# Kernel optimization log

Hardware: AMD Instinct MI355X
Metric: run time of the kernel (lower is better)

The kernel has to match this reference:

```python
import jax, jax.numpy as jnp
import numpy as np

B, L, D_IN, H, FEAT, PROJ = 1024, 128, 130, 768, 49, 40


def setup_inputs() -> dict:
    key = jax.random.key(0)
    ks = jax.random.split(key, 16)
    s = 0.05
    return {
        "X": jax.random.normal(ks[0], (B, L, D_IN), dtype=jnp.float32),
        "Fe": jax.random.normal(ks[1], (B, FEAT), dtype=jnp.float32),
        # three attention heads densa1/2/3 stacked: [3, H, L]
        "W_att": jax.random.normal(ks[2], (3, H, L), dtype=jnp.float32) * s,
        "b_att": jax.random.normal(ks[3], (3, L), dtype=jnp.float32) * s,
        # LSTMCell(3*D_IN, H) params, PyTorch layout
        "W_ih": jax.random.normal(ks[4], (4 * H, 3 * D_IN), dtype=jnp.float32) * s,
        "W_hh": jax.random.normal(ks[5], (4 * H, H), dtype=jnp.float32) * s,
        "b_ih": jax.random.normal(ks[6], (4 * H,), dtype=jnp.float32) * s,
        "b_hh": jax.random.normal(ks[7], (4 * H,), dtype=jnp.float32) * s,
        # Dense1: Linear(H, FEAT)
        "W_d1": jax.random.normal(ks[8], (FEAT, H), dtype=jnp.float32) * s,
        "b_d1": jax.random.normal(ks[9], (FEAT,), dtype=jnp.float32) * s,
        # AttFeat R: Linear(FEAT, PROJ); A: Linear(PROJ, 1, bias=False)
        "W_r": jax.random.normal(ks[10], (PROJ, FEAT), dtype=jnp.float32) * s,
        "b_r": jax.random.normal(ks[11], (PROJ,), dtype=jnp.float32) * s,
        "W_a": jax.random.normal(ks[12], (1, PROJ), dtype=jnp.float32) * s,
        # Dense2: Linear(PROJ, 2)
        "W_d2": jax.random.normal(ks[13], (2, PROJ), dtype=jnp.float32) * s,
        "b_d2": jax.random.normal(ks[14], (2,), dtype=jnp.float32) * s,
    }


def reference(X, Fe, W_att, b_att, W_ih, W_hh, b_ih, b_hh, W_d1, b_d1, W_r, b_r, W_a, W_d2, b_d2):
    b = X.shape[0]

    def step(carry, _):
        h, c = carry
        # three softmax attention distributions over the sequence: [b, 3, L]
        logits = jnp.einsum('bh,khl->bkl', h, W_att) + b_att
        alp = jax.nn.softmax(logits, axis=-1)
        # weighted sums over seq -> concat of v1,v2,v3: [b, 3*D_IN]
        v = jnp.einsum('bkl,bld->bkd', alp, X).reshape(b, -1)
        # PyTorch LSTMCell update
        gates = v @ W_ih.T + b_ih + h @ W_hh.T + b_hh
        i, f, g, o = jnp.split(gates, 4, axis=-1)
        c_new = jax.nn.sigmoid(f) * c + jax.nn.sigmoid(i) * jnp.tanh(g)
        h_new = jax.nn.sigmoid(o) * jnp.tanh(c_new)
        return (h_new, c_new), h_new

    h0 = jnp.zeros((b, H), dtype=X.dtype)
    c0 = jnp.zeros((b, H), dtype=X.dtype)
    _, hs = jax.lax.scan(step, (h0, c0), None, length=L)  # [L, b, H]
    out = jnp.transpose(hs, (1, 0, 2))                    # [b, L, H]

    # MaxLayer: max-pool over the sequence dim
    x = jnp.max(out, axis=1)                              # [b, H]

    # Dense1 + ReLU
    y = jax.nn.relu(x @ W_d1.T + b_d1)                    # [b, FEAT]

    # AttFeat over [y, Fe]
    r1 = jax.nn.leaky_relu(y @ W_r.T + b_r)               # [b, PROJ]
    r2 = jax.nn.leaky_relu(Fe @ W_r.T + b_r)
    a1 = jnp.tanh(r1) @ W_a.T                             # [b, 1]
    a2 = jnp.tanh(r2) @ W_a.T
    a = jax.nn.softmax(jnp.concatenate([a1, a2], axis=-1), axis=-1)  # [b, 2]
    s = jax.nn.relu(a[:, 0:1] * r1 + a[:, 1:2] * r2)      # [b, PROJ]

    # Dense2 (squeeze is a no-op for b > 1)
    return s @ W_d2.T + b_d2                              # [b, 2]
```

## Files before the change

kernel.cpp:

```cpp
#include <hip/hip_runtime.h>
#include <stdint.h>


#define B_SZ   1024
#define LSEQ   128
#define DIN    130
#define HDIM   768
#define NFEAT  49
#define NPROJ  40
#define KPAD   1216
#define VOFF   416
#define NGATE  3072
#define KT_G   19
#define XELEM  (LSEQ * DIN)
#define GBUF   20480

typedef unsigned short u16;
typedef __attribute__((ext_vector_type(8))) short short8;
typedef __attribute__((ext_vector_type(4))) float f32x4;

__device__ __forceinline__ u16 f2bf(float f) {
  unsigned int u = __float_as_uint(f);
  u += 0x7FFFu + ((u >> 16) & 1u);
  return (u16)(u >> 16);
}
__device__ __forceinline__ float bf2f(u16 b) {
  return __uint_as_float(((unsigned int)b) << 16);
}
__device__ __forceinline__ float frcp(float x) {
  return __builtin_amdgcn_rcpf(x);
}
__device__ __forceinline__ float ftanh(float x) {
  return 1.f - 2.f * frcp(1.f + __expf(2.f * x));
}
__device__ __forceinline__ float fsigm(float x) {
  return frcp(1.f + __expf(-x));
}
__device__ __forceinline__ void gload16(const void* g, void* l) {
  __builtin_amdgcn_global_load_lds(
      (__attribute__((address_space(1))) const void*)g,
      (__attribute__((address_space(3))) void*)l, 16, 0, 0);
}

__global__ __launch_bounds__(256, 4) void gemm_logits_k(
    const u16* __restrict__ Ah,
    const u16* __restrict__ Bh, float* __restrict__ Cp)
{
  __shared__ __align__(16) u16 sAh[32 * 40];
  __shared__ __align__(16) u16 sBh[64 * 40];

  const int tid = threadIdx.x, lane = tid & 63, wid = tid >> 6;
  const int wm = (wid & 1) * 16, wn = (wid >> 1) * 32;
  const int lm = lane & 15, quad = lane >> 4;
  const int bm = blockIdx.x * 32, bn = blockIdx.y * 64;
  const int kh = blockIdx.z;
  const int kbase = kh * 384;
  float* __restrict__ C = Cp + (size_t)kh * B_SZ * 384;

  const bool aload = tid < 128;
  const int ar = tid >> 2, ac = (tid & 3) * 8;
  const size_t a_off = (size_t)(bm + ar) * KPAD + kbase + ac;
  const size_t b_off = (size_t)(bn + ar) * HDIM + kbase + ac;

  uint4 ph, pb;
  if (aload) ph = *(const uint4*)(Ah + a_off);
  pb = *(const uint4*)(Bh + b_off);

  f32x4 acc0 = {0.f, 0.f, 0.f, 0.f}, acc1 = {0.f, 0.f, 0.f, 0.f};

  for (int kt = 0; kt < 12; ++kt) {
    if (aload) *(uint4*)&sAh[ar * 40 + ac] = ph;
    *(uint4*)&sBh[ar * 40 + ac] = pb;
    __syncthreads();
    if (kt + 1 < 12) {
      const int k0 = (kt + 1) * 32;
      if (aload) ph = *(const uint4*)(Ah + a_off + k0);
      pb = *(const uint4*)(Bh + b_off + k0);
    }
    const short8 ah = *(const short8*)&sAh[(wm + lm) * 40 + quad * 8];
    const short8 b0 = *(const short8*)&sBh[(wn + lm) * 40 + quad * 8];
    const short8 b1 = *(const short8*)&sBh[(wn + 16 + lm) * 40 + quad * 8];
    acc0 = __builtin_amdgcn_mfma_f32_16x16x32_bf16(ah, b0, acc0, 0, 0, 0);
    acc1 = __builtin_amdgcn_mfma_f32_16x16x32_bf16(ah, b1, acc1, 0, 0, 0);
    __syncthreads();
  }

  const int col = bn + wn + lm;
  const int row0 = bm + wm + quad * 4;
#pragma unroll
  for (int r = 0; r < 4; ++r) {
    C[(size_t)(row0 + r) * 384 + col]      = acc0[r];
    C[(size_t)(row0 + r) * 384 + col + 16] = acc1[r];
  }
}

__global__ __launch_bounds__(256, 2) void gates_lstm(
    const u16* __restrict__ Ah,
    const u16* __restrict__ Wh,
    const float* __restrict__ bsum,
    float* __restrict__ cst, float* __restrict__ hmax,
    u16* __restrict__ out_h)
{
  __shared__ __align__(16) char smem[3 * GBUF];

  const int tid = threadIdx.x, lane = tid & 63, wid = tid >> 6;
  const int wm = (wid >> 1) * 32, wn = (wid & 1) * 48;
  const int lm = lane & 15, quad = lane >> 4;

  const int wg = blockIdx.x;
  const int vid = (wg & 7) * 64 + (wg >> 3);
  const int bm = (vid & 15) * 64;
  const int j0 = (vid >> 4) * 24;

  const u16* Asrc[2];
#pragma unroll
  for (int i = 0; i < 2; ++i) {
    const int r = i * 32 + wid * 8 + (lane >> 3);
    const int s = (lane & 7) ^ (r & 7);
    Asrc[i] = Ah + (size_t)(bm + r) * KPAD + (s << 3);
  }
  const u16* Bsrc[3];
#pragma unroll
  for (int i = 0; i < 3; ++i) {
    const int r = i * 32 + wid * 8 + (lane >> 3);
    const int s = (lane & 7) ^ (r & 7);
    const int nrow = (r / 24) * HDIM + j0 + (r % 24);
    Bsrc[i] = Wh + (size_t)nrow * KPAD + (s << 3);
  }

  int aoff[2], boff[3];
#pragma unroll
  for (int mi = 0; mi < 2; ++mi) {
    const int R = wm + mi * 16 + lm;
    aoff[mi] = R * 64 + ((quad ^ (R & 7)) << 3);
  }
#pragma unroll
  for (int ni = 0; ni < 3; ++ni) {
    const int R = wn + ni * 16 + lm;
    boff[ni] = R * 64 + ((quad ^ (R & 7)) << 3);
  }

  f32x4 acc[2][3];
#pragma unroll
  for (int mi = 0; mi < 2; ++mi)
#pragma unroll
    for (int ni = 0; ni < 3; ++ni) acc[mi][ni] = (f32x4){0.f, 0.f, 0.f, 0.f};

  auto stage = [&](int buf, int kt) {
    char* bb = smem + buf * GBUF;
    const int k0 = kt * 64;
#pragma unroll
    for (int i = 0; i < 2; ++i)
      gload16(Asrc[i] + k0, bb + ((i << 12) + (wid << 10)));
#pragma unroll
    for (int i = 0; i < 3; ++i)
      gload16(Bsrc[i] + k0, bb + 8192 + ((i << 12) + (wid << 10)));
  };

  stage(0, 0);
  stage(1, 1);

  int cur = 0;
  for (int kt = 0; kt < KT_G; ++kt) {
    if (kt + 2 < KT_G) {
      int nbuf = cur + 2; if (nbuf >= 3) nbuf -= 3;
      stage(nbuf, kt + 2);
      asm volatile("s_waitcnt vmcnt(10)" ::: "memory");
    } else if (kt + 1 < KT_G) {
      asm volatile("s_waitcnt vmcnt(5)" ::: "memory");
    } else {
      asm volatile("s_waitcnt vmcnt(0)" ::: "memory");
    }
    asm volatile("s_barrier" ::: "memory");

    const u16* sA = (const u16*)(smem + cur * GBUF);
    const u16* sB = sA + 4096;
#pragma unroll
    for (int kk = 0; kk < 2; ++kk) {
      const int kx = kk << 5;
      short8 af[2], bg[3];
#pragma unroll
      for (int mi = 0; mi < 2; ++mi)
        af[mi] = *(const short8*)(sA + (aoff[mi] ^ kx));
#pragma unroll
      for (int ni = 0; ni < 3; ++ni)
        bg[ni] = *(const short8*)(sB + (boff[ni] ^ kx));
#pragma unroll
      for (int mi = 0; mi < 2; ++mi)
#pragma unroll
        for (int ni = 0; ni < 3; ++ni)
          acc[mi][ni] = __builtin_amdgcn_mfma_f32_16x16x32_bf16(
              af[mi], bg[ni], acc[mi][ni], 0, 0, 0);
    }
    asm volatile("s_barrier" ::: "memory");
    cur += 1; if (cur >= 3) cur -= 3;
  }

  float* tile = (float*)smem;
#pragma unroll
  for (int mi = 0; mi < 2; ++mi)
#pragma unroll
    for (int ni = 0; ni < 3; ++ni) {
      const int c = wn + ni * 16 + lm;
#pragma unroll
      for (int r = 0; r < 4; ++r)
        tile[(wm + mi * 16 + quad * 4 + r) * 100 + c] = acc[mi][ni][r];
    }
  __syncthreads();

#pragma unroll
  for (int i = 0; i < 6; ++i) {
    const int lin = tid + 256 * i;
    const int row = lin / 24, jj = lin - row * 24;
    const int b = bm + row, j = j0 + jj;
    const float* tr = tile + row * 100;
    const float pi = tr[jj]      + bsum[j];
    const float pf = tr[24 + jj] + bsum[HDIM + j];
    const float pg = tr[48 + jj] + bsum[2 * HDIM + j];
    const float po = tr[72 + jj] + bsum[3 * HDIM + j];
    const float si = fsigm(pi);
    const float sf = fsigm(pf);
    const float so = fsigm(po);
    const size_t cidx = (size_t)b * HDIM + j;
    const float cn = sf * cst[cidx] + si * ftanh(pg);
    const float hn = so * ftanh(cn);
    cst[cidx] = cn;
    hmax[cidx] = fmaxf(hmax[cidx], hn);
    out_h[(size_t)b * KPAD + VOFF + j] = f2bf(hn);
  }
}

__global__ __launch_bounds__(512, 4) void softmax_v(
    const float* __restrict__ l0, const float* __restrict__ l1,
    const float* __restrict__ b_att,
    const u16* __restrict__ XT,
    u16* __restrict__ act)
{
  const int b = blockIdx.x;
  const int t = threadIdx.x;
  __shared__ __align__(16) u16 sXT[XELEM];
  __shared__ __align__(16) float s_alp[384];
  __shared__ float s_w[16];

  {
    const uint4* src = (const uint4*)(XT + (size_t)b * XELEM);
    uint4* dst = (uint4*)sXT;
#pragma unroll
    for (int rep = 0; rep < 4; ++rep) {
      const int i = t + rep * 512;
      const int d = i >> 4, blk = i & 15;
      dst[d * 16 + (blk ^ (d & 7))] = src[i];
    }
    if (t < 32) {
      const int i = 2048 + t;
      const int d = i >> 4, blk = i & 15;
      dst[d * 16 + (blk ^ (d & 7))] = src[i];
    }
  }

  const int lane = t & 63, wv = t >> 6, hw = wv & ~1;
  float x = -3.4e38f;
  if (t < 384)
    x = l0[(size_t)b * 384 + t] + l1[(size_t)b * 384 + t] + b_att[t];

  float m = x;
#pragma unroll
  for (int off = 32; off > 0; off >>= 1) m = fmaxf(m, __shfl_xor(m, off));
  if (lane == 0 && wv < 6) s_w[wv] = m;
  __syncthreads();

  float e = 0.f;
  if (t < 384) e = __expf(x - fmaxf(s_w[hw], s_w[hw | 1]));
  float sum = e;
#pragma unroll
  for (int off = 32; off > 0; off >>= 1) sum += __shfl_xor(sum, off);
  if (lane == 0 && wv < 6) s_w[8 + wv] = sum;
  __syncthreads();

  if (t < 384) {
    const float sk = s_w[8 + hw] + s_w[8 + (hw | 1)];
    s_alp[t] = e * frcp(sk);
  }
  __syncthreads();

  if (t < 390) {
    const int k = t / 130;
    const int d = t - k * 130;
    const uint4* xr = (const uint4*)sXT;
    const int dbase = d * 16, dsw = d & 7;
    const float* ab = s_alp + (k << 7);
    float acc = 0.f;
#pragma unroll
    for (int c = 0; c < 16; ++c) {
      const uint4 raw = xr[dbase + (c ^ dsw)];
      const float4 a0 = *(const float4*)(ab + (c << 3));
      const float4 a1 = *(const float4*)(ab + (c << 3) + 4);
      acc += a0.x * bf2f((u16)(raw.x & 0xffff));
      acc += a0.y * bf2f((u16)(raw.x >> 16));
      acc += a0.z * bf2f((u16)(raw.y & 0xffff));
      acc += a0.w * bf2f((u16)(raw.y >> 16));
      acc += a1.x * bf2f((u16)(raw.z & 0xffff));
      acc += a1.y * bf2f((u16)(raw.z >> 16));
      acc += a1.z * bf2f((u16)(raw.w & 0xffff));
      acc += a1.w * bf2f((u16)(raw.w >> 16));
    }
    act[(size_t)b * KPAD + t] = f2bf(acc);
  }
}

__global__ __launch_bounds__(64) void final_head(
    const float* __restrict__ hmax, const float* __restrict__ Fe,
    const float* __restrict__ W_d1, const float* __restrict__ b_d1,
    const float* __restrict__ W_r,  const float* __restrict__ b_r,
    const float* __restrict__ W_a,
    const float* __restrict__ W_d2, const float* __restrict__ b_d2,
    float* __restrict__ out)
{
  const int b = blockIdx.x;
  const int t = threadIdx.x;
  __shared__ float sx[HDIM];
  __shared__ float sy[NFEAT];
  __shared__ float sr1[NPROJ], sr2[NPROJ];
  __shared__ float sa[2];

  for (int i = t; i < HDIM; i += 64) sx[i] = hmax[(size_t)b * HDIM + i];
  __syncthreads();

  if (t < NFEAT) {
    float acc = b_d1[t];
    const float* w = W_d1 + (size_t)t * HDIM;
    for (int i = 0; i < HDIM; ++i) acc += sx[i] * w[i];
    sy[t] = fmaxf(acc, 0.f);
  }
  __syncthreads();

  if (t < NPROJ) {
    float a1 = b_r[t], a2 = b_r[t];
    const float* w  = W_r + (size_t)t * NFEAT;
    const float* fe = Fe + (size_t)b * NFEAT;
    for (int i = 0; i < NFEAT; ++i) { a1 += sy[i] * w[i]; a2 += fe[i] * w[i]; }
    sr1[t] = (a1 > 0.f) ? a1 : 0.01f * a1;
    sr2[t] = (a2 > 0.f) ? a2 : 0.01f * a2;
  }
  __syncthreads();

  if (t == 0) {
    float a1 = 0.f, a2 = 0.f;
    for (int p = 0; p < NPROJ; ++p) {
      a1 += tanhf(sr1[p]) * W_a[p];
      a2 += tanhf(sr2[p]) * W_a[p];
    }
    const float mx = fmaxf(a1, a2);
    const float e1 = expf(a1 - mx), e2 = expf(a2 - mx);
    sa[0] = e1 / (e1 + e2);
    sa[1] = e2 / (e1 + e2);
  }
  __syncthreads();

  if (t < 2) {
    float acc = b_d2[t];
    const float* w = W_d2 + (size_t)t * NPROJ;
    for (int p = 0; p < NPROJ; ++p) {
      float s = sa[0] * sr1[p] + sa[1] * sr2[p];
      s = fmaxf(s, 0.f);
      acc += s * w[p];
    }
    out[(size_t)b * 2 + t] = acc;
  }
}

__global__ __launch_bounds__(256) void pack_w(
    const float* __restrict__ W_ih, const float* __restrict__ W_hh,
    const float* __restrict__ b_ih, const float* __restrict__ b_hh,
    u16* __restrict__ hi, float* __restrict__ bsum)
{
  const int idx = blockIdx.x * 256 + threadIdx.x;
  if (idx >= NGATE * KPAD) return;
  const int n = idx / KPAD;
  const int k = idx - n * KPAD;
  float v = 0.f;
  if (k < 3 * DIN)                       v = W_ih[(size_t)n * (3 * DIN) + k];
  else if (k >= VOFF && k < VOFF + HDIM) v = W_hh[(size_t)n * HDIM + (k - VOFF)];
  hi[idx] = f2bf(v);
  if (k == 0) bsum[n] = b_ih[n] + b_hh[n];
}

__global__ __launch_bounds__(256) void pack_watt(
    const float* __restrict__ W_att,
    u16* __restrict__ hi)
{
  const int idx = blockIdx.x * 256 + threadIdx.x;
  if (idx >= 384 * HDIM) return;
  const int n = idx / HDIM;
  const int h = idx - n * HDIM;
  const int katt = n >> 7;
  const int l = n & 127;
  hi[idx] = f2bf(W_att[((size_t)katt * HDIM + h) * LSEQ + l]);
}

__global__ __launch_bounds__(256) void pack_xt(
    const float* __restrict__ X, u16* __restrict__ XT)
{
  const int b = blockIdx.x;
  const int t = threadIdx.x;
  __shared__ u16 sX[XELEM];
  const float* src = X + (size_t)b * XELEM;
  for (int i = t; i < XELEM; i += 256) sX[i] = f2bf(src[i]);
  __syncthreads();
  uint4* dst = (uint4*)(XT + (size_t)b * XELEM);
  for (int u = t; u < 2080; u += 256) {
    const int d = u >> 4, blk = u & 15;
    const int lb = blk * 8;
    ushort4 w0, w1;
    w0.x = sX[(lb + 0) * DIN + d]; w0.y = sX[(lb + 1) * DIN + d];
    w0.z = sX[(lb + 2) * DIN + d]; w0.w = sX[(lb + 3) * DIN + d];
    w1.x = sX[(lb + 4) * DIN + d]; w1.y = sX[(lb + 5) * DIN + d];
    w1.z = sX[(lb + 6) * DIN + d]; w1.w = sX[(lb + 7) * DIN + d];
    uint4 o;
    o.x = (unsigned)w0.x | ((unsigned)w0.y << 16);
    o.y = (unsigned)w0.z | ((unsigned)w0.w << 16);
    o.z = (unsigned)w1.x | ((unsigned)w1.y << 16);
    o.w = (unsigned)w1.z | ((unsigned)w1.w << 16);
    dst[u] = o;
  }
}

__global__ __launch_bounds__(256) void init_state(
    u16* __restrict__ a0, u16* __restrict__ a1,
    float* __restrict__ cst, float* __restrict__ hmax)
{
  const int idx = blockIdx.x * 256 + threadIdx.x;
  if (idx < B_SZ * KPAD) { a0[idx] = 0; a1[idx] = 0; }
  if (idx < B_SZ * HDIM) { cst[idx] = 0.f; hmax[idx] = -3.4e38f; }
}

extern "C" void kernel_launch(void* const* d_in, const int* in_sizes, int n_in,
                              void* d_out, int out_size, void* d_ws, size_t ws_size,
                              hipStream_t stream) {
  const float* X     = (const float*)d_in[0];
  const float* Fe    = (const float*)d_in[1];
  const float* W_att = (const float*)d_in[2];
  const float* b_att = (const float*)d_in[3];
  const float* W_ih  = (const float*)d_in[4];
  const float* W_hh  = (const float*)d_in[5];
  const float* b_ih  = (const float*)d_in[6];
  const float* b_hh  = (const float*)d_in[7];
  const float* W_d1  = (const float*)d_in[8];
  const float* b_d1  = (const float*)d_in[9];
  const float* W_r   = (const float*)d_in[10];
  const float* b_r   = (const float*)d_in[11];
  const float* W_a   = (const float*)d_in[12];
  const float* W_d2  = (const float*)d_in[13];
  const float* b_d2  = (const float*)d_in[14];
  float* out = (float*)d_out;

  char* base = (char*)d_ws;
  size_t off = 0;
  auto alloc = [&](size_t nbytes) -> void* {
    void* p = base + off;
    off = (off + nbytes + 255) & ~(size_t)255;
    return p;
  };
  u16* act0    = (u16*)alloc((size_t)B_SZ * KPAD * 2);
  u16* act1    = (u16*)alloc((size_t)B_SZ * KPAD * 2);
  u16* wcat    = (u16*)alloc((size_t)NGATE * KPAD * 2);
  u16* watt    = (u16*)alloc((size_t)384 * HDIM * 2);
  u16* xt16    = (u16*)alloc((size_t)B_SZ * XELEM * 2);
  float* bsum  = (float*)alloc((size_t)NGATE * 4);
  float* lpart = (float*)alloc((size_t)2 * B_SZ * 384 * 4);
  float* cst   = (float*)alloc((size_t)B_SZ * HDIM * 4);
  float* hmax  = (float*)alloc((size_t)B_SZ * HDIM * 4);

  pack_w<<<(NGATE * KPAD + 255) / 256, 256, 0, stream>>>(W_ih, W_hh, b_ih, b_hh, wcat, bsum);
  pack_watt<<<(384 * HDIM + 255) / 256, 256, 0, stream>>>(W_att, watt);
  pack_xt<<<B_SZ, 256, 0, stream>>>(X, xt16);
  init_state<<<(B_SZ * KPAD + 255) / 256, 256, 0, stream>>>(act0, act1, cst, hmax);

  float* l0 = lpart;
  float* l1 = lpart + (size_t)B_SZ * 384;

  gemm_logits_k<<<dim3(B_SZ / 32, 384 / 64, 2), 256, 0, stream>>>(act0 + VOFF, watt, lpart);
  softmax_v<<<B_SZ, 512, 0, stream>>>(l0, l1, b_att, xt16, act0);

  u16 *rd = act0, *wr = act1;
  for (int step = 0; step < LSEQ; ++step) {
    gates_lstm<<<dim3(512), 256, 0, stream>>>(rd, wcat, bsum, cst, hmax, wr);
    if (step + 1 < LSEQ) {
      gemm_logits_k<<<dim3(B_SZ / 32, 384 / 64, 2), 256, 0, stream>>>(wr + VOFF, watt, lpart);
      softmax_v<<<B_SZ, 512, 0, stream>>>(l0, l1, b_att, xt16, wr);
    }
    u16* tt = rd; rd = wr; wr = tt;
  }

  final_head<<<B_SZ, 64, 0, stream>>>(hmax, Fe, W_d1, b_d1, W_r, b_r, W_a, W_d2, b_d2, out);
}
```

Baseline: 4.206 ms.

## Fuse attention-logit GEMM into LSTM gate kernel epilogue via split-K partials

Removes the separate logits GEMM launch per step. Each gates_lstm block now multiplies its freshly computed 64x24 bf16 h slice by the matching 24-column slice of W_att held in LDS, and writes per-slice partial logits into a 32-way split buffer. softmax_v then sums the 32 partials per element. This saves one launch and the re-read of h every step. In exchange it writes and reads a much larger partial buffer (32x B x 384 floats) and adds LDS work and registers to the gate kernel.

```diff
diff --git a/kernel.cpp b/kernel.cpp
--- a/kernel.cpp
+++ b/kernel.cpp
@@ -8,6 +8,7 @@
 #define HDIM   768
 #define NFEAT  49
 #define NPROJ  40
+#define NATT   384
 #define KPAD   1216
 #define VOFF   416
 #define NGATE  3072
@@ -42,64 +43,14 @@
       (__attribute__((address_space(3))) void*)l, 16, 0, 0);
 }
 
-__global__ __launch_bounds__(256, 4) void gemm_logits_k(
-    const u16* __restrict__ Ah,
-    const u16* __restrict__ Bh, float* __restrict__ Cp)
-{
-  __shared__ __align__(16) u16 sAh[32 * 40];
-  __shared__ __align__(16) u16 sBh[64 * 40];
-
-  const int tid = threadIdx.x, lane = tid & 63, wid = tid >> 6;
-  const int wm = (wid & 1) * 16, wn = (wid >> 1) * 32;
-  const int lm = lane & 15, quad = lane >> 4;
-  const int bm = blockIdx.x * 32, bn = blockIdx.y * 64;
-  const int kh = blockIdx.z;
-  const int kbase = kh * 384;
-  float* __restrict__ C = Cp + (size_t)kh * B_SZ * 384;
-
-  const bool aload = tid < 128;
-  const int ar = tid >> 2, ac = (tid & 3) * 8;
-  const size_t a_off = (size_t)(bm + ar) * KPAD + kbase + ac;
-  const size_t b_off = (size_t)(bn + ar) * HDIM + kbase + ac;
-
-  uint4 ph, pb;
-  if (aload) ph = *(const uint4*)(Ah + a_off);
-  pb = *(const uint4*)(Bh + b_off);
-
-  f32x4 acc0 = {0.f, 0.f, 0.f, 0.f}, acc1 = {0.f, 0.f, 0.f, 0.f};
-
-  for (int kt = 0; kt < 12; ++kt) {
-    if (aload) *(uint4*)&sAh[ar * 40 + ac] = ph;
-    *(uint4*)&sBh[ar * 40 + ac] = pb;
-    __syncthreads();
-    if (kt + 1 < 12) {
-      const int k0 = (kt + 1) * 32;
-      if (aload) ph = *(const uint4*)(Ah + a_off + k0);
-      pb = *(const uint4*)(Bh + b_off + k0);
-    }
-    const short8 ah = *(const short8*)&sAh[(wm + lm) * 40 + quad * 8];
-    const short8 b0 = *(const short8*)&sBh[(wn + lm) * 40 + quad * 8];
-    const short8 b1 = *(const short8*)&sBh[(wn + 16 + lm) * 40 + quad * 8];
-    acc0 = __builtin_amdgcn_mfma_f32_16x16x32_bf16(ah, b0, acc0, 0, 0, 0);
-    acc1 = __builtin_amdgcn_mfma_f32_16x16x32_bf16(ah, b1, acc1, 0, 0, 0);
-    __syncthreads();
-  }
-
-  const int col = bn + wn + lm;
-  const int row0 = bm + wm + quad * 4;
-#pragma unroll
-  for (int r = 0; r < 4; ++r) {
-    C[(size_t)(row0 + r) * 384 + col]      = acc0[r];
-    C[(size_t)(row0 + r) * 384 + col + 16] = acc1[r];
-  }
-}
-
 __global__ __launch_bounds__(256, 2) void gates_lstm(
     const u16* __restrict__ Ah,
     const u16* __restrict__ Wh,
+    const u16* __restrict__ watt,
     const float* __restrict__ bsum,
     float* __restrict__ cst, float* __restrict__ hmax,
-    u16* __restrict__ out_h)
+    u16* __restrict__ out_h,
+    float* __restrict__ lpart)
 {
   __shared__ __align__(16) char smem[3 * GBUF];
 
@@ -110,7 +61,8 @@
   const int wg = blockIdx.x;
   const int vid = (wg & 7) * 64 + (wg >> 3);
   const int bm = (vid & 15) * 64;
-  const int j0 = (vid >> 4) * 24;
+  const int js = vid >> 4;
+  const int j0 = js * 24;
 
   const u16* Asrc[2];
 #pragma unroll
@@ -197,6 +149,9 @@
   }
 
   float* tile = (float*)smem;
+  u16* sH = (u16*)(smem + 25600);
+  u16* sW = (u16*)(smem + 30720);
+
 #pragma unroll
   for (int mi = 0; mi < 2; ++mi)
 #pragma unroll
@@ -206,6 +161,27 @@
       for (int r = 0; r < 4; ++r)
         tile[(wm + mi * 16 + quad * 4 + r) * 100 + c] = acc[mi][ni][r];
     }
+  {
+    const int row = tid >> 2, c4 = tid & 3;
+    *(ushort4*)&sH[row * 40 + 24 + c4 * 4] = (ushort4){0, 0, 0, 0};
+  }
+#pragma unroll
+  for (int i = 0; i < 5; ++i) {
+    const int idx = tid + 256 * i;
+    if (idx < 1152) {
+      const int row = idx / 3, c = idx - row * 3;
+      *(uint4*)&sW[row * 40 + c * 8] =
+          *(const uint4*)(watt + (size_t)row * HDIM + j0 + c * 8);
+    }
+  }
+#pragma unroll
+  for (int i = 0; i < 2; ++i) {
+    const int row = tid + 256 * i;
+    if (row < NATT) {
+      *(uint4*)&sW[row * 40 + 24] = (uint4){0, 0, 0, 0};
+      *(uint4*)&sW[row * 40 + 32] = (uint4){0, 0, 0, 0};
+    }
+  }
   __syncthreads();
 
 #pragma unroll
@@ -226,15 +202,50 @@
     const float hn = so * ftanh(cn);
     cst[cidx] = cn;
     hmax[cidx] = fmaxf(hmax[cidx], hn);
-    out_h[(size_t)b * KPAD + VOFF + j] = f2bf(hn);
+    const u16 hb = f2bf(hn);
+    out_h[(size_t)b * KPAD + VOFF + j] = hb;
+    sH[row * 40 + jj] = hb;
+  }
+  __syncthreads();
+
+  {
+    const int n0 = wid * 96;
+    short8 ah2[4];
+#pragma unroll
+    for (int mi = 0; mi < 4; ++mi)
+      ah2[mi] = *(const short8*)&sH[(mi * 16 + lm) * 40 + quad * 8];
+    f32x4 ac2[4][6];
+#pragma unroll
+    for (int mi = 0; mi < 4; ++mi)
+#pragma unroll
+      for (int ni = 0; ni < 6; ++ni) ac2[mi][ni] = (f32x4){0.f, 0.f, 0.f, 0.f};
+#pragma unroll
+    for (int ni = 0; ni < 6; ++ni) {
+      const short8 bw = *(const short8*)&sW[(n0 + ni * 16 + lm) * 40 + quad * 8];
+#pragma unroll
+      for (int mi = 0; mi < 4; ++mi)
+        ac2[mi][ni] = __builtin_amdgcn_mfma_f32_16x16x32_bf16(
+            ah2[mi], bw, ac2[mi][ni], 0, 0, 0);
+    }
+    float* lp = lpart + (size_t)js * B_SZ * NATT;
+#pragma unroll
+    for (int mi = 0; mi < 4; ++mi)
+#pragma unroll
+      for (int ni = 0; ni < 6; ++ni) {
+        const int col = n0 + ni * 16 + lm;
+        const int row0 = bm + mi * 16 + quad * 4;
+#pragma unroll
+        for (int r = 0; r < 4; ++r)
+          lp[(size_t)(row0 + r) * NATT + col] = ac2[mi][ni][r];
+      }
   }
 }
 
 __global__ __launch_bounds__(512, 4) void softmax_v(
-    const float* __restrict__ l0, const float* __restrict__ l1,
+    const float* __restrict__ lpart,
     const float* __restrict__ b_att,
     const u16* __restrict__ XT,
-    u16* __restrict__ act)
+    u16* __restrict__ act, int np)
 {
   const int b = blockIdx.x;
   const int t = threadIdx.x;
@@ -260,8 +271,17 @@
 
   const int lane = t & 63, wv = t >> 6, hw = wv & ~1;
   float x = -3.4e38f;
-  if (t < 384)
-    x = l0[(size_t)b * 384 + t] + l1[(size_t)b * 384 + t] + b_att[t];
+  if (t < 384) {
+    float s0 = 0.f, s1 = 0.f, s2 = 0.f, s3 = 0.f;
+    const float* lp = lpart + t + (size_t)b * NATT;
+    for (int p = 0; p + 3 < np; p += 4) {
+      s0 += lp[(size_t)(p + 0) * B_SZ * NATT];
+      s1 += lp[(size_t)(p + 1) * B_SZ * NATT];
+      s2 += lp[(size_t)(p + 2) * B_SZ * NATT];
+      s3 += lp[(size_t)(p + 3) * B_SZ * NATT];
+    }
+    x = b_att[t] + ((s0 + s1) + (s2 + s3));
+  }
 
   float m = x;
 #pragma unroll
@@ -390,7 +410,7 @@
     u16* __restrict__ hi)
 {
   const int idx = blockIdx.x * 256 + threadIdx.x;
-  if (idx >= 384 * HDIM) return;
+  if (idx >= NATT * HDIM) return;
   const int n = idx / HDIM;
   const int h = idx - n * HDIM;
   const int katt = n >> 7;
@@ -464,30 +484,25 @@
   u16* act0    = (u16*)alloc((size_t)B_SZ * KPAD * 2);
   u16* act1    = (u16*)alloc((size_t)B_SZ * KPAD * 2);
   u16* wcat    = (u16*)alloc((size_t)NGATE * KPAD * 2);
-  u16* watt    = (u16*)alloc((size_t)384 * HDIM * 2);
+  u16* watt    = (u16*)alloc((size_t)NATT * HDIM * 2);
   u16* xt16    = (u16*)alloc((size_t)B_SZ * XELEM * 2);
   float* bsum  = (float*)alloc((size_t)NGATE * 4);
-  float* lpart = (float*)alloc((size_t)2 * B_SZ * 384 * 4);
+  float* lp32  = (float*)alloc((size_t)32 * B_SZ * NATT * 4);
   float* cst   = (float*)alloc((size_t)B_SZ * HDIM * 4);
   float* hmax  = (float*)alloc((size_t)B_SZ * HDIM * 4);
 
   pack_w<<<(NGATE * KPAD + 255) / 256, 256, 0, stream>>>(W_ih, W_hh, b_ih, b_hh, wcat, bsum);
-  pack_watt<<<(384 * HDIM + 255) / 256, 256, 0, stream>>>(W_att, watt);
+  pack_watt<<<(NATT * HDIM + 255) / 256, 256, 0, stream>>>(W_att, watt);
   pack_xt<<<B_SZ, 256, 0, stream>>>(X, xt16);
   init_state<<<(B_SZ * KPAD + 255) / 256, 256, 0, stream>>>(act0, act1, cst, hmax);
 
-  float* l0 = lpart;
-  float* l1 = lpart + (size_t)B_SZ * 384;
-
-  gemm_logits_k<<<dim3(B_SZ / 32, 384 / 64, 2), 256, 0, stream>>>(act0 + VOFF, watt, lpart);
-  softmax_v<<<B_SZ, 512, 0, stream>>>(l0, l1, b_att, xt16, act0);
+  softmax_v<<<B_SZ, 512, 0, stream>>>(lp32, b_att, xt16, act0, 0);
 
   u16 *rd = act0, *wr = act1;
   for (int step = 0; step < LSEQ; ++step) {
-    gates_lstm<<<dim3(512), 256, 0, stream>>>(rd, wcat, bsum, cst, hmax, wr);
+    gates_lstm<<<dim3(512), 256, 0, stream>>>(rd, wcat, watt, bsum, cst, hmax, wr, lp32);
     if (step + 1 < LSEQ) {
-      gemm_logits_k<<<dim3(B_SZ / 32, 384 / 64, 2), 256, 0, stream>>>(wr + VOFF, watt, lpart);
-      softmax_v<<<B_SZ, 512, 0, stream>>>(l0, l1, b_att, xt16, wr);
+      softmax_v<<<B_SZ, 512, 0, stream>>>(lp32, b_att, xt16, wr, 32);
     }
     u16* tt = rd; rd = wr; wr = tt;
   }
```

Result: slower. 5.168 ms (+22.9%).
